# Kernel tuning notes

Hardware: AMD Instinct MI355X
Metric: run time of the kernel (lower is better)

The kernel has to match this reference:

```python
import jax, jax.numpy as jnp
import numpy as np

HID = 768
HEADS = 12
HEAD_LEN = HID // HEADS
SCALE_INV = 1.0 / np.sqrt(HEAD_LEN).astype(np.float32)


def setup_inputs() -> dict:
    key = jax.random.key(0)
    ks = jax.random.split(key, 5)
    std = 1.0 / np.sqrt(HID)
    return {
        "x": jax.random.normal(ks[0], (1, 4096, HID), dtype=jnp.float32),
        "w_q": jax.random.normal(ks[1], (HID, HID), dtype=jnp.float32) * std,
        "w_k": jax.random.normal(ks[2], (HID, HID), dtype=jnp.float32) * std,
        "w_v": jax.random.normal(ks[3], (HID, HID), dtype=jnp.float32) * std,
        "w_fc": jax.random.normal(ks[4], (HID, HID), dtype=jnp.float32) * std,
    }


def reference(x, w_q, w_k, w_v, w_fc):
    B, S, D = x.shape
    # torch Linear weight layout [out, in]: y = x @ W.T
    def proj_heads(w):
        y = jnp.einsum("bsd,ed->bse", x, w)
        return y.reshape(B, S, HEADS, HEAD_LEN).transpose(0, 2, 1, 3)  # bhsd
    q = proj_heads(w_q)
    k = proj_heads(w_k)
    v = proj_heads(w_v)
    scores = SCALE_INV * jnp.einsum("bhqd,bhkd->bhqk", q, k)
    attn = jax.nn.softmax(scores, axis=-1)
    out = jnp.einsum("bhqk,bhkd->bhqd", attn, v)
    out = out.transpose(0, 2, 1, 3).reshape(B, S, D)
    return jnp.einsum("bsd,ed->bse", out, w_fc)
```

## Files before the change

kernel.cpp:

```cpp
#include <hip/hip_runtime.h>
#include <hip/hip_bf16.h>

#define S_LEN 4096
#define HID 768
#define NHEAD 12
#define HL 64

typedef __attribute__((ext_vector_type(8))) short short8;
typedef __attribute__((ext_vector_type(4))) float f32x4;
using bf16 = __hip_bfloat16;

__device__ __forceinline__ void gl2lds16(const void* g, void* l) {
  __builtin_amdgcn_global_load_lds((__attribute__((address_space(1))) void*)(g),
                                   (__attribute__((address_space(3))) void*)(l),
                                   16, 0, 0);
}

__device__ __forceinline__ f32x4 mfma_bf16(short8 a, short8 b, f32x4 c) {
  return __builtin_amdgcn_mfma_f32_16x16x32_bf16(a, b, c, 0, 0, 0);
}

__device__ __forceinline__ void storeC(float* C, long idx, float v) { C[idx] = v; }
__device__ __forceinline__ void storeC(bf16* C, long idx, float v) { C[idx] = __float2bfloat16(v); }

#define BAR() asm volatile("s_waitcnt lgkmcnt(0)\n\ts_barrier" ::: "memory")

__global__ __launch_bounds__(256) void cvt_all(
    const float* __restrict__ x, const float* __restrict__ wq,
    const float* __restrict__ wk, const float* __restrict__ wv,
    const float* __restrict__ wfc, bf16* __restrict__ xb, bf16* __restrict__ wqb,
    bf16* __restrict__ wkb, bf16* __restrict__ wvb, bf16* __restrict__ wfcb) {
  const long NX = (long)S_LEN * HID;
  const long NW = (long)HID * HID;
  long i = ((long)blockIdx.x * 256 + threadIdx.x) * 4;
  const float* src;
  bf16* dst;
  long off;
  if (i < NX) {
    src = x; dst = xb; off = i;
  } else {
    long j = i - NX;
    int wsel = (int)(j / NW);
    off = j - (long)wsel * NW;
    src = wsel == 0 ? wq : wsel == 1 ? wk : wsel == 2 ? wv : wfc;
    dst = wsel == 0 ? wqb : wsel == 1 ? wkb : wsel == 2 ? wvb : wfcb;
  }
  float4 v = *(const float4*)(src + off);
  bf16 h0 = __float2bfloat16(v.x), h1 = __float2bfloat16(v.y);
  bf16 h2 = __float2bfloat16(v.z), h3 = __float2bfloat16(v.w);
  ushort4 o;
  o.x = *(unsigned short*)&h0; o.y = *(unsigned short*)&h1;
  o.z = *(unsigned short*)&h2; o.w = *(unsigned short*)&h3;
  *(ushort4*)(dst + off) = o;
}

template <typename OT>
__global__ __launch_bounds__(256) void gemm_bt(
    const bf16* __restrict__ A, const bf16* __restrict__ B0,
    const bf16* __restrict__ B1, const bf16* __restrict__ B2,
    OT* __restrict__ C0, OT* __restrict__ C1, OT* __restrict__ C2, float qscale) {
  constexpr int K = HID;
  __shared__ __align__(16) bf16 As[128 * 32];
  __shared__ __align__(16) bf16 Bs[128 * 32];
  const int z = blockIdx.z;
  const bf16* B = (z == 0) ? B0 : (z == 1) ? B1 : B2;
  OT* C = (z == 0) ? C0 : (z == 1) ? C1 : C2;
  const float sc = (z == 0) ? qscale : 1.0f;
  const int bm = blockIdx.y, bn = blockIdx.x;
  const int t = threadIdx.x, lane = t & 63, w = t >> 6;
  const int wm = w >> 1, wn = w & 1;
  const int q4 = lane >> 4, c16 = lane & 15;
  const int srow = lane >> 2, scol = (lane & 3) * 8;
  const bf16* Ab = A + (long)bm * 128 * K;
  const bf16* Bb = B + (long)bn * 128 * K;
  f32x4 acc[4][4] = {};
  for (int k0 = 0; k0 < K; k0 += 32) {
#pragma unroll
    for (int r = 0; r < 2; ++r) {
      int rowb = r * 64 + w * 16;
      gl2lds16(Ab + (long)(rowb + srow) * K + k0 + scol, &As[rowb * 32]);
      gl2lds16(Bb + (long)(rowb + srow) * K + k0 + scol, &Bs[rowb * 32]);
    }
    __syncthreads();
    short8 af[4], bfv[4];
#pragma unroll
    for (int i = 0; i < 4; ++i)
      af[i] = *(const short8*)&As[(wm * 64 + i * 16 + c16) * 32 + q4 * 8];
#pragma unroll
    for (int j = 0; j < 4; ++j)
      bfv[j] = *(const short8*)&Bs[(wn * 64 + j * 16 + c16) * 32 + q4 * 8];
#pragma unroll
    for (int i = 0; i < 4; ++i)
#pragma unroll
      for (int j = 0; j < 4; ++j)
        acc[i][j] = mfma_bf16(af[i], bfv[j], acc[i][j]);
    __syncthreads();
  }
  const long crow0 = (long)bm * 128 + wm * 64;
  const int ccol0 = bn * 128 + wn * 64;
#pragma unroll
  for (int i = 0; i < 4; ++i)
#pragma unroll
    for (int j = 0; j < 4; ++j)
#pragma unroll
      for (int r = 0; r < 4; ++r) {
        long row = crow0 + i * 16 + q4 * 4 + r;
        int col = ccol0 + j * 16 + c16;
        storeC(C, row * HID + col, sc * acc[i][j][r]);
      }
}

__global__ __launch_bounds__(256) void gemm_fc(const bf16* __restrict__ A,
                                               const bf16* __restrict__ B,
                                               float* __restrict__ C) {
  __shared__ __align__(16) bf16 As[128 * 32];
  __shared__ __align__(16) bf16 Bs[64 * 32];
  const int bm = blockIdx.y, bn = blockIdx.x;
  const int t = threadIdx.x, lane = t & 63, w = t >> 6;
  const int q4 = lane >> 4, c16 = lane & 15;
  const int srow = lane >> 2, scol = (lane & 3) * 8;
  const bf16* Ab = A + (long)bm * 128 * HID;
  const bf16* Bb = B + (long)bn * 64 * HID;
  f32x4 acc[2][4] = {};
  for (int k0 = 0; k0 < HID; k0 += 32) {
#pragma unroll
    for (int r = 0; r < 2; ++r) {
      int rowb = w * 32 + r * 16;
      gl2lds16(Ab + (long)(rowb + srow) * HID + k0 + scol, &As[rowb * 32]);
    }
    gl2lds16(Bb + (long)(w * 16 + srow) * HID + k0 + scol, &Bs[w * 16 * 32]);
    __syncthreads();
    short8 af[2], bfv[4];
#pragma unroll
    for (int i = 0; i < 2; ++i)
      af[i] = *(const short8*)&As[(w * 32 + i * 16 + c16) * 32 + q4 * 8];
#pragma unroll
    for (int j = 0; j < 4; ++j)
      bfv[j] = *(const short8*)&Bs[(j * 16 + c16) * 32 + q4 * 8];
#pragma unroll
    for (int i = 0; i < 2; ++i)
#pragma unroll
      for (int j = 0; j < 4; ++j)
        acc[i][j] = mfma_bf16(af[i], bfv[j], acc[i][j]);
    __syncthreads();
  }
#pragma unroll
  for (int i = 0; i < 2; ++i)
#pragma unroll
    for (int j = 0; j < 4; ++j)
#pragma unroll
      for (int r = 0; r < 4; ++r) {
        long row = (long)bm * 128 + w * 32 + i * 16 + q4 * 4 + r;
        int col = bn * 64 + j * 16 + c16;
        C[row * HID + col] = acc[i][j][r];
      }
}

__global__ __launch_bounds__(256) void transpose_v(const bf16* __restrict__ V,
                                                   bf16* __restrict__ Vt) {
  __shared__ unsigned short tile[64][65];
  const int bs = blockIdx.x * 64;
  const int be = blockIdx.y * 64;
  const int t = threadIdx.x;
#pragma unroll
  for (int p = 0; p < 4; ++p) {
    int i = p * 256 + t;
    int r = i >> 4;
    int c = (i & 15) * 4;
    ushort4 v = *(const ushort4*)((const unsigned short*)V + (long)(bs + r) * HID + be + c);
    tile[r][c] = v.x; tile[r][c + 1] = v.y; tile[r][c + 2] = v.z; tile[r][c + 3] = v.w;
  }
  __syncthreads();
#pragma unroll
  for (int p = 0; p < 4; ++p) {
    int i = p * 256 + t;
    int r = i >> 4;
    int c = (i & 15) * 4;
    ushort4 v;
    v.x = tile[c][r]; v.y = tile[c + 1][r]; v.z = tile[c + 2][r]; v.w = tile[c + 3][r];
    *(ushort4*)((unsigned short*)Vt + (long)(be + r) * S_LEN + bs + c) = v;
  }
}

__global__ __launch_bounds__(256, 3) void flash_attn(const bf16* __restrict__ Q,
                                                     const bf16* __restrict__ Kg,
                                                     const bf16* __restrict__ Vt,
                                                     bf16* __restrict__ O) {
  __shared__ __align__(16) bf16 Ps[2][64 * 128];
  __shared__ float Lred[4][64];
  const int qt = blockIdx.x, h = blockIdx.y;
  const int t = threadIdx.x, lane = t & 63, w = t >> 6;
  const int q4 = lane >> 4, c16 = lane & 15;
  const int s0 = qt * 64;

  short8 qf[2][4];
  {
    const bf16* Qb = Q + (long)(s0 + c16) * HID + h * HL + q4 * 8;
#pragma unroll
    for (int j = 0; j < 4; ++j)
#pragma unroll
      for (int ks = 0; ks < 2; ++ks)
        qf[ks][j] = *(const short8*)(Qb + (long)j * 16 * HID + ks * 32);
  }
  const bf16* kp = Kg + (long)(w * 32 + c16) * HID + h * HL + q4 * 8;
  const bf16* vp = Vt + (long)(h * HL + w * 16 + c16) * S_LEN + q4 * 8;

  float l_part[4] = {0.f, 0.f, 0.f, 0.f};
  f32x4 o_acc[4] = {};
  short8 kf[2][2], vf[4];
#pragma unroll
  for (int rr = 0; rr < 2; ++rr)
#pragma unroll
    for (int ks = 0; ks < 2; ++ks)
      kf[rr][ks] = *(const short8*)(kp + (long)rr * 16 * HID + ks * 32);
#pragma unroll
  for (int kc = 0; kc < 4; ++kc) vf[kc] = *(const short8*)(vp + kc * 32);

  for (int kt = 0; kt < S_LEN / 128; ++kt) {
    bf16* Pb = Ps[kt & 1];
    f32x4 sacc[2][4] = {};
#pragma unroll
    for (int rr = 0; rr < 2; ++rr)
#pragma unroll
      for (int ks = 0; ks < 2; ++ks)
#pragma unroll
        for (int j = 0; j < 4; ++j)
          sacc[rr][j] = mfma_bf16(kf[rr][ks], qf[ks][j], sacc[rr][j]);

    const bf16* kpn = (kt == S_LEN / 128 - 1) ? kp : kp + 128 * HID;
#pragma unroll
    for (int rr = 0; rr < 2; ++rr)
#pragma unroll
      for (int ks = 0; ks < 2; ++ks)
        kf[rr][ks] = *(const short8*)(kpn + (long)rr * 16 * HID + ks * 32);
    kp = kpn;

#pragma unroll
    for (int rr = 0; rr < 2; ++rr) {
      const int wch = ((w * 4 + rr * 2 + (q4 >> 1)));
#pragma unroll
      for (int j = 0; j < 4; ++j) {
        float p0 = __builtin_amdgcn_exp2f(sacc[rr][j][0]);
        float p1 = __builtin_amdgcn_exp2f(sacc[rr][j][1]);
        float p2 = __builtin_amdgcn_exp2f(sacc[rr][j][2]);
        float p3 = __builtin_amdgcn_exp2f(sacc[rr][j][3]);
        l_part[j] += (p0 + p1) + (p2 + p3);
        __hip_bfloat162 a01 = __float22bfloat162_rn(float2{p0, p1});
        __hip_bfloat162 a23 = __float22bfloat162_rn(float2{p2, p3});
        int2 pk;
        pk.x = *(int*)&a01;
        pk.y = *(int*)&a23;
        *(int2*)&Pb[(j * 16 + c16) * 128 + (wch ^ c16) * 8 + (q4 & 1) * 4] = pk;
      }
    }
    BAR();

#pragma unroll
    for (int kc = 0; kc < 4; ++kc) {
#pragma unroll
      for (int j = 0; j < 4; ++j) {
        short8 pf = *(const short8*)&Pb[(j * 16 + c16) * 128 + ((kc * 4 + q4) ^ c16) * 8];
        o_acc[j] = mfma_bf16(vf[kc], pf, o_acc[j]);
      }
    }
    const bf16* vpn = (kt == S_LEN / 128 - 1) ? vp : vp + 128;
#pragma unroll
    for (int kc = 0; kc < 4; ++kc) vf[kc] = *(const short8*)(vpn + kc * 32);
    vp = vpn;
  }

#pragma unroll
  for (int j = 0; j < 4; ++j) {
    float s = l_part[j];
    s += __shfl_xor(s, 16, 64);
    s += __shfl_xor(s, 32, 64);
    Lred[w][j * 16 + c16] = s;
  }
  __syncthreads();
#pragma unroll
  for (int j = 0; j < 4; ++j) {
    int q = j * 16 + c16;
    float lt = Lred[0][q] + Lred[1][q] + Lred[2][q] + Lred[3][q];
    float rl = 1.0f / lt;
    float v0 = o_acc[j][0] * rl, v1 = o_acc[j][1] * rl;
    float v2 = o_acc[j][2] * rl, v3 = o_acc[j][3] * rl;
    bf16 b0 = __float2bfloat16(v0), b1 = __float2bfloat16(v1);
    bf16 b2 = __float2bfloat16(v2), b3 = __float2bfloat16(v3);
    short4 pk;
    pk.x = *(short*)&b0; pk.y = *(short*)&b1; pk.z = *(short*)&b2; pk.w = *(short*)&b3;
    *(short4*)&O[(long)(s0 + q) * HID + h * HL + w * 16 + q4 * 4] = pk;
  }
}

extern "C" void kernel_launch(void* const* d_in, const int* in_sizes, int n_in,
                              void* d_out, int out_size, void* d_ws, size_t ws_size,
                              hipStream_t stream) {
  const float* x = (const float*)d_in[0];
  const float* wq = (const float*)d_in[1];
  const float* wk = (const float*)d_in[2];
  const float* wv = (const float*)d_in[3];
  const float* wfc = (const float*)d_in[4];
  float* out = (float*)d_out;

  const long NBIG = (long)S_LEN * HID * sizeof(bf16);
  const long NWB = (long)HID * HID * sizeof(bf16);
  char* p = (char*)d_ws;
  bf16* xb = (bf16*)p;   p += NBIG;
  bf16* wqb = (bf16*)p;  p += NWB;
  bf16* wkb = (bf16*)p;  p += NWB;
  bf16* wvb = (bf16*)p;  p += NWB;
  bf16* wfcb = (bf16*)p; p += NWB;
  bf16* Qb = (bf16*)p;   p += NBIG;
  bf16* Kb = (bf16*)p;   p += NBIG;
  bf16* Vb = (bf16*)p;   p += NBIG;
  bf16* Vtb = (bf16*)p;  p += NBIG;
  bf16* Ob = (bf16*)p;   p += NBIG;

  const float c1 = 0.125f * 1.44269504088896340736f;

  const long total4 = ((long)S_LEN * HID + 4L * HID * HID) / 4;
  cvt_all<<<(int)(total4 / 256), 256, 0, stream>>>(x, wq, wk, wv, wfc, xb, wqb, wkb,
                                                   wvb, wfcb);
  gemm_bt<bf16><<<dim3(HID / 128, S_LEN / 128, 3), 256, 0, stream>>>(
      xb, wqb, wkb, wvb, Qb, Kb, Vb, c1);
  transpose_v<<<dim3(S_LEN / 64, HID / 64), 256, 0, stream>>>(Vb, Vtb);
  flash_attn<<<dim3(S_LEN / 64, NHEAD), 256, 0, stream>>>(Qb, Kb, Vtb, Ob);
  gemm_fc<<<dim3(HID / 64, S_LEN / 128), 256, 0, stream>>>(Ob, wfcb, out);
}
```

Before: 211.0 us.

## Triple-buffer LDS in projection GEMMs with async prefetch and smaller fc tiles

Both bf16 GEMMs now keep three LDS buffers and issue global-to-LDS loads two k-steps ahead. Each step uses a single barrier that waits on vmcnt instead of two __syncthreads, so loads can overlap MFMA work. The output GEMM also switches to 64x64 tiles on a 2x2 wave grid, doubling its block count for better CU coverage. The cost is more LDS per block and a hand-tuned vmcnt wait count that has to match the number of outstanding loads.

```diff
diff --git a/kernel.cpp b/kernel.cpp
--- a/kernel.cpp
+++ b/kernel.cpp
@@ -24,6 +24,8 @@
 __device__ __forceinline__ void storeC(bf16* C, long idx, float v) { C[idx] = __float2bfloat16(v); }
 
 #define BAR() asm volatile("s_waitcnt lgkmcnt(0)\n\ts_barrier" ::: "memory")
+#define BAR_VM(n) \
+  asm volatile("s_waitcnt vmcnt(" #n ") lgkmcnt(0)\n\ts_barrier" ::: "memory")
 
 __global__ __launch_bounds__(256) void cvt_all(
     const float* __restrict__ x, const float* __restrict__ wq,
@@ -55,13 +57,13 @@
 }
 
 template <typename OT>
-__global__ __launch_bounds__(256) void gemm_bt(
+__global__ __launch_bounds__(256, 3) void gemm_bt(
     const bf16* __restrict__ A, const bf16* __restrict__ B0,
     const bf16* __restrict__ B1, const bf16* __restrict__ B2,
     OT* __restrict__ C0, OT* __restrict__ C1, OT* __restrict__ C2, float qscale) {
-  constexpr int K = HID;
-  __shared__ __align__(16) bf16 As[128 * 32];
-  __shared__ __align__(16) bf16 Bs[128 * 32];
+  constexpr int K = HID, NK = K / 32;
+  __shared__ __align__(16) bf16 As[3][128 * 32];
+  __shared__ __align__(16) bf16 Bs[3][128 * 32];
   const int z = blockIdx.z;
   const bf16* B = (z == 0) ? B0 : (z == 1) ? B1 : B2;
   OT* C = (z == 0) ? C0 : (z == 1) ? C1 : C2;
@@ -73,28 +75,36 @@
   const int srow = lane >> 2, scol = (lane & 3) * 8;
   const bf16* Ab = A + (long)bm * 128 * K;
   const bf16* Bb = B + (long)bn * 128 * K;
-  f32x4 acc[4][4] = {};
-  for (int k0 = 0; k0 < K; k0 += 32) {
+
+  auto stage = [&](int k, int buf) {
 #pragma unroll
     for (int r = 0; r < 2; ++r) {
       int rowb = r * 64 + w * 16;
-      gl2lds16(Ab + (long)(rowb + srow) * K + k0 + scol, &As[rowb * 32]);
-      gl2lds16(Bb + (long)(rowb + srow) * K + k0 + scol, &Bs[rowb * 32]);
+      gl2lds16(Ab + (long)(rowb + srow) * K + k * 32 + scol, &As[buf][rowb * 32]);
+      gl2lds16(Bb + (long)(rowb + srow) * K + k * 32 + scol, &Bs[buf][rowb * 32]);
     }
-    __syncthreads();
+  };
+
+  f32x4 acc[4][4] = {};
+  stage(0, 0);
+  stage(1, 1);
+  for (int k = 0; k < NK; ++k) {
+    if (k < NK - 1) BAR_VM(4); else BAR_VM(0);
+    if (k + 2 < NK) stage(k + 2, (k + 2) % 3);
+    const bf16* Al = As[k % 3];
+    const bf16* Bl = Bs[k % 3];
     short8 af[4], bfv[4];
 #pragma unroll
     for (int i = 0; i < 4; ++i)
-      af[i] = *(const short8*)&As[(wm * 64 + i * 16 + c16) * 32 + q4 * 8];
+      af[i] = *(const short8*)&Al[(wm * 64 + i * 16 + c16) * 32 + q4 * 8];
 #pragma unroll
     for (int j = 0; j < 4; ++j)
-      bfv[j] = *(const short8*)&Bs[(wn * 64 + j * 16 + c16) * 32 + q4 * 8];
+      bfv[j] = *(const short8*)&Bl[(wn * 64 + j * 16 + c16) * 32 + q4 * 8];
 #pragma unroll
     for (int i = 0; i < 4; ++i)
 #pragma unroll
       for (int j = 0; j < 4; ++j)
         acc[i][j] = mfma_bf16(af[i], bfv[j], acc[i][j]);
-    __syncthreads();
   }
   const long crow0 = (long)bm * 128 + wm * 64;
   const int ccol0 = bn * 128 + wn * 64;
@@ -110,48 +120,56 @@
       }
 }
 
-__global__ __launch_bounds__(256) void gemm_fc(const bf16* __restrict__ A,
-                                               const bf16* __restrict__ B,
-                                               float* __restrict__ C) {
-  __shared__ __align__(16) bf16 As[128 * 32];
-  __shared__ __align__(16) bf16 Bs[64 * 32];
+__global__ __launch_bounds__(256, 3) void gemm_fc(const bf16* __restrict__ A,
+                                                  const bf16* __restrict__ B,
+                                                  float* __restrict__ C) {
+  constexpr int NK = HID / 32;
+  __shared__ __align__(16) bf16 As[3][64 * 32];
+  __shared__ __align__(16) bf16 Bs[3][64 * 32];
   const int bm = blockIdx.y, bn = blockIdx.x;
   const int t = threadIdx.x, lane = t & 63, w = t >> 6;
+  const int wm = w >> 1, wn = w & 1;
   const int q4 = lane >> 4, c16 = lane & 15;
   const int srow = lane >> 2, scol = (lane & 3) * 8;
-  const bf16* Ab = A + (long)bm * 128 * HID;
+  const bf16* Ab = A + (long)bm * 64 * HID;
   const bf16* Bb = B + (long)bn * 64 * HID;
-  f32x4 acc[2][4] = {};
-  for (int k0 = 0; k0 < HID; k0 += 32) {
-#pragma unroll
-    for (int r = 0; r < 2; ++r) {
-      int rowb = w * 32 + r * 16;
-      gl2lds16(Ab + (long)(rowb + srow) * HID + k0 + scol, &As[rowb * 32]);
-    }
-    gl2lds16(Bb + (long)(w * 16 + srow) * HID + k0 + scol, &Bs[w * 16 * 32]);
-    __syncthreads();
-    short8 af[2], bfv[4];
+
+  auto stage = [&](int k, int buf) {
+    gl2lds16(Ab + (long)(w * 16 + srow) * HID + k * 32 + scol,
+             &As[buf][w * 16 * 32]);
+    gl2lds16(Bb + (long)(w * 16 + srow) * HID + k * 32 + scol,
+             &Bs[buf][w * 16 * 32]);
+  };
+
+  f32x4 acc[2][2] = {};
+  stage(0, 0);
+  stage(1, 1);
+  for (int k = 0; k < NK; ++k) {
+    if (k < NK - 1) BAR_VM(2); else BAR_VM(0);
+    if (k + 2 < NK) stage(k + 2, (k + 2) % 3);
+    const bf16* Al = As[k % 3];
+    const bf16* Bl = Bs[k % 3];
+    short8 af[2], bfv[2];
 #pragma unroll
     for (int i = 0; i < 2; ++i)
-      af[i] = *(const short8*)&As[(w * 32 + i * 16 + c16) * 32 + q4 * 8];
-#pragma unroll
-    for (int j = 0; j < 4; ++j)
-      bfv[j] = *(const short8*)&Bs[(j * 16 + c16) * 32 + q4 * 8];
+      af[i] = *(const short8*)&Al[(wm * 32 + i * 16 + c16) * 32 + q4 * 8];
+#pragma unroll
+    for (int j = 0; j < 2; ++j)
+      bfv[j] = *(const short8*)&Bl[(wn * 32 + j * 16 + c16) * 32 + q4 * 8];
 #pragma unroll
     for (int i = 0; i < 2; ++i)
 #pragma unroll
-      for (int j = 0; j < 4; ++j)
+      for (int j = 0; j < 2; ++j)
         acc[i][j] = mfma_bf16(af[i], bfv[j], acc[i][j]);
-    __syncthreads();
   }
 #pragma unroll
   for (int i = 0; i < 2; ++i)
 #pragma unroll
-    for (int j = 0; j < 4; ++j)
+    for (int j = 0; j < 2; ++j)
 #pragma unroll
       for (int r = 0; r < 4; ++r) {
-        long row = (long)bm * 128 + w * 32 + i * 16 + q4 * 4 + r;
-        int col = bn * 64 + j * 16 + c16;
+        long row = (long)bm * 64 + wm * 32 + i * 16 + q4 * 4 + r;
+        int col = bn * 64 + wn * 32 + j * 16 + c16;
         C[row * HID + col] = acc[i][j][r];
       }
 }
@@ -325,5 +343,5 @@
       xb, wqb, wkb, wvb, Qb, Kb, Vb, c1);
   transpose_v<<<dim3(S_LEN / 64, HID / 64), 256, 0, stream>>>(Vb, Vtb);
   flash_attn<<<dim3(S_LEN / 64, NHEAD), 256, 0, stream>>>(Qb, Kb, Vtb, Ob);
-  gemm_fc<<<dim3(HID / 64, S_LEN / 128), 256, 0, stream>>>(Ob, wfcb, out);
-}
+  gemm_fc<<<dim3(HID / 64, S_LEN / 64), 256, 0, stream>>>(Ob, wfcb, out);
+}
```

Result: no change. 213.3 us (+1.1%).

## Fuse all stages into one persistent kernel with software grid barriers

Applied to the files above, without the earlier changes.

Merges the conversion, QKV projection, V transpose, flash attention and output projection into a single 768-block kernel separated by atomic-counter grid barriers. It removes launch gaps and the separate transpose pass by writing V transposed from the projection epilogue through LDS. GEMM tiles are retiled (128x96 for QKV, 64x64 for FC) to match the fixed block count. The software grid barrier needs all 768 blocks co-resident (3 per CU at launch bounds 3), which could deadlock if occupancy falls short, and the smaller FC tiles reduce data reuse.

```diff
diff --git a/kernel.cpp b/kernel.cpp
--- a/kernel.cpp
+++ b/kernel.cpp
@@ -5,6 +5,7 @@
 #define HID 768
 #define NHEAD 12
 #define HL 64
+#define NBLK 768u
 
 typedef __attribute__((ext_vector_type(8))) short short8;
 typedef __attribute__((ext_vector_type(4))) float f32x4;
@@ -20,275 +21,283 @@
   return __builtin_amdgcn_mfma_f32_16x16x32_bf16(a, b, c, 0, 0, 0);
 }
 
-__device__ __forceinline__ void storeC(float* C, long idx, float v) { C[idx] = v; }
-__device__ __forceinline__ void storeC(bf16* C, long idx, float v) { C[idx] = __float2bfloat16(v); }
-
 #define BAR() asm volatile("s_waitcnt lgkmcnt(0)\n\ts_barrier" ::: "memory")
 
-__global__ __launch_bounds__(256) void cvt_all(
+__device__ __forceinline__ void gridbar(unsigned* cnt, int idx) {
+  __syncthreads();
+  __threadfence();
+  if (threadIdx.x == 0) {
+    atomicAdd(&cnt[idx], 1u);
+    while (__hip_atomic_load(&cnt[idx], __ATOMIC_RELAXED,
+                             __HIP_MEMORY_SCOPE_AGENT) < NBLK)
+      __builtin_amdgcn_s_sleep(8);
+  }
+  __syncthreads();
+  __threadfence();
+}
+
+__global__ __launch_bounds__(256, 3) void mha_mega(
     const float* __restrict__ x, const float* __restrict__ wq,
     const float* __restrict__ wk, const float* __restrict__ wv,
-    const float* __restrict__ wfc, bf16* __restrict__ xb, bf16* __restrict__ wqb,
-    bf16* __restrict__ wkb, bf16* __restrict__ wvb, bf16* __restrict__ wfcb) {
-  const long NX = (long)S_LEN * HID;
-  const long NW = (long)HID * HID;
-  long i = ((long)blockIdx.x * 256 + threadIdx.x) * 4;
-  const float* src;
-  bf16* dst;
-  long off;
-  if (i < NX) {
-    src = x; dst = xb; off = i;
-  } else {
-    long j = i - NX;
-    int wsel = (int)(j / NW);
-    off = j - (long)wsel * NW;
-    src = wsel == 0 ? wq : wsel == 1 ? wk : wsel == 2 ? wv : wfc;
-    dst = wsel == 0 ? wqb : wsel == 1 ? wkb : wsel == 2 ? wvb : wfcb;
-  }
-  float4 v = *(const float4*)(src + off);
-  bf16 h0 = __float2bfloat16(v.x), h1 = __float2bfloat16(v.y);
-  bf16 h2 = __float2bfloat16(v.z), h3 = __float2bfloat16(v.w);
-  ushort4 o;
-  o.x = *(unsigned short*)&h0; o.y = *(unsigned short*)&h1;
-  o.z = *(unsigned short*)&h2; o.w = *(unsigned short*)&h3;
-  *(ushort4*)(dst + off) = o;
-}
-
-template <typename OT>
-__global__ __launch_bounds__(256) void gemm_bt(
-    const bf16* __restrict__ A, const bf16* __restrict__ B0,
-    const bf16* __restrict__ B1, const bf16* __restrict__ B2,
-    OT* __restrict__ C0, OT* __restrict__ C1, OT* __restrict__ C2, float qscale) {
-  constexpr int K = HID;
-  __shared__ __align__(16) bf16 As[128 * 32];
-  __shared__ __align__(16) bf16 Bs[128 * 32];
-  const int z = blockIdx.z;
-  const bf16* B = (z == 0) ? B0 : (z == 1) ? B1 : B2;
-  OT* C = (z == 0) ? C0 : (z == 1) ? C1 : C2;
-  const float sc = (z == 0) ? qscale : 1.0f;
-  const int bm = blockIdx.y, bn = blockIdx.x;
-  const int t = threadIdx.x, lane = t & 63, w = t >> 6;
-  const int wm = w >> 1, wn = w & 1;
-  const int q4 = lane >> 4, c16 = lane & 15;
-  const int srow = lane >> 2, scol = (lane & 3) * 8;
-  const bf16* Ab = A + (long)bm * 128 * K;
-  const bf16* Bb = B + (long)bn * 128 * K;
-  f32x4 acc[4][4] = {};
-  for (int k0 = 0; k0 < K; k0 += 32) {
-#pragma unroll
-    for (int r = 0; r < 2; ++r) {
-      int rowb = r * 64 + w * 16;
-      gl2lds16(Ab + (long)(rowb + srow) * K + k0 + scol, &As[rowb * 32]);
-      gl2lds16(Bb + (long)(rowb + srow) * K + k0 + scol, &Bs[rowb * 32]);
-    }
-    __syncthreads();
-    short8 af[4], bfv[4];
-#pragma unroll
-    for (int i = 0; i < 4; ++i)
-      af[i] = *(const short8*)&As[(wm * 64 + i * 16 + c16) * 32 + q4 * 8];
-#pragma unroll
-    for (int j = 0; j < 4; ++j)
-      bfv[j] = *(const short8*)&Bs[(wn * 64 + j * 16 + c16) * 32 + q4 * 8];
-#pragma unroll
-    for (int i = 0; i < 4; ++i)
-#pragma unroll
-      for (int j = 0; j < 4; ++j)
-        acc[i][j] = mfma_bf16(af[i], bfv[j], acc[i][j]);
-    __syncthreads();
-  }
-  const long crow0 = (long)bm * 128 + wm * 64;
-  const int ccol0 = bn * 128 + wn * 64;
-#pragma unroll
-  for (int i = 0; i < 4; ++i)
-#pragma unroll
-    for (int j = 0; j < 4; ++j)
-#pragma unroll
-      for (int r = 0; r < 4; ++r) {
-        long row = crow0 + i * 16 + q4 * 4 + r;
-        int col = ccol0 + j * 16 + c16;
-        storeC(C, row * HID + col, sc * acc[i][j][r]);
-      }
-}
-
-__global__ __launch_bounds__(256) void gemm_fc(const bf16* __restrict__ A,
-                                               const bf16* __restrict__ B,
-                                               float* __restrict__ C) {
-  __shared__ __align__(16) bf16 As[128 * 32];
-  __shared__ __align__(16) bf16 Bs[64 * 32];
-  const int bm = blockIdx.y, bn = blockIdx.x;
+    const float* __restrict__ wfc, bf16* __restrict__ xb,
+    bf16* __restrict__ wqb, bf16* __restrict__ wkb, bf16* __restrict__ wvb,
+    bf16* __restrict__ wfcb, bf16* __restrict__ Qb, bf16* __restrict__ Kb,
+    bf16* __restrict__ Vtb, bf16* __restrict__ Ob, float* __restrict__ out,
+    unsigned* __restrict__ cnt) {
+  __shared__ __align__(16) char SMEM[33792];
+  const int b = blockIdx.x;
   const int t = threadIdx.x, lane = t & 63, w = t >> 6;
   const int q4 = lane >> 4, c16 = lane & 15;
-  const int srow = lane >> 2, scol = (lane & 3) * 8;
-  const bf16* Ab = A + (long)bm * 128 * HID;
-  const bf16* Bb = B + (long)bn * 64 * HID;
-  f32x4 acc[2][4] = {};
-  for (int k0 = 0; k0 < HID; k0 += 32) {
-#pragma unroll
-    for (int r = 0; r < 2; ++r) {
-      int rowb = w * 32 + r * 16;
-      gl2lds16(Ab + (long)(rowb + srow) * HID + k0 + scol, &As[rowb * 32]);
-    }
-    gl2lds16(Bb + (long)(w * 16 + srow) * HID + k0 + scol, &Bs[w * 16 * 32]);
+  const float c1 = 0.125f * 1.44269504088896340736f;
+
+  {
+    const long NX4 = (long)S_LEN * HID / 4;
+    const long NW4 = (long)HID * HID / 4;
+#pragma unroll
+    for (int i = 0; i < 7; ++i) {
+      long g = (long)i * 196608 + (long)b * 256 + t;
+      const float4* src;
+      ushort4* dst;
+      long off;
+      if (g < NX4) {
+        src = (const float4*)x; dst = (ushort4*)xb; off = g;
+      } else {
+        long j = g - NX4;
+        int zz = (int)(j / NW4);
+        off = j - (long)zz * NW4;
+        src = (const float4*)(zz == 0 ? wq : zz == 1 ? wk : zz == 2 ? wv : wfc);
+        dst = (ushort4*)(zz == 0 ? wqb : zz == 1 ? wkb : zz == 2 ? wvb : wfcb);
+      }
+      float4 v = src[off];
+      bf16 h0 = __float2bfloat16(v.x), h1 = __float2bfloat16(v.y);
+      bf16 h2 = __float2bfloat16(v.z), h3 = __float2bfloat16(v.w);
+      ushort4 o;
+      o.x = *(unsigned short*)&h0; o.y = *(unsigned short*)&h1;
+      o.z = *(unsigned short*)&h2; o.w = *(unsigned short*)&h3;
+      dst[off] = o;
+    }
+  }
+  gridbar(cnt, 0);
+
+  {
+    bf16* As = (bf16*)SMEM;
+    bf16* Bs = (bf16*)(SMEM + 128 * 32 * 2);
+    const int z = b >> 8, r8 = b & 255, bn = r8 & 7, bm = r8 >> 3;
+    const bf16* A = xb + (long)bm * 128 * HID;
+    const bf16* Bw = (z == 0 ? wqb : z == 1 ? wkb : wvb) + (long)bn * 96 * HID;
+    const int wm = w >> 1, wn = w & 1;
+    const int srow = lane >> 2, scol = (lane & 3) * 8;
+    f32x4 acc[4][3] = {};
+    for (int k0 = 0; k0 < HID; k0 += 32) {
+      gl2lds16(A + (long)(w * 16 + srow) * HID + k0 + scol, &As[w * 16 * 32]);
+      gl2lds16(A + (long)(64 + w * 16 + srow) * HID + k0 + scol,
+               &As[(64 + w * 16) * 32]);
+      gl2lds16(Bw + (long)(w * 16 + srow) * HID + k0 + scol, &Bs[w * 16 * 32]);
+      if (w < 2)
+        gl2lds16(Bw + (long)(64 + w * 16 + srow) * HID + k0 + scol,
+                 &Bs[(64 + w * 16) * 32]);
+      __syncthreads();
+      short8 af[4], bfv[3];
+#pragma unroll
+      for (int i = 0; i < 4; ++i)
+        af[i] = *(const short8*)&As[(wm * 64 + i * 16 + c16) * 32 + q4 * 8];
+#pragma unroll
+      for (int j = 0; j < 3; ++j)
+        bfv[j] = *(const short8*)&Bs[(wn * 48 + j * 16 + c16) * 32 + q4 * 8];
+#pragma unroll
+      for (int i = 0; i < 4; ++i)
+#pragma unroll
+        for (int j = 0; j < 3; ++j)
+          acc[i][j] = mfma_bf16(af[i], bfv[j], acc[i][j]);
+      __syncthreads();
+    }
+    if (z < 2) {
+      bf16* C = (z == 0) ? Qb : Kb;
+      const float sc = (z == 0) ? c1 : 1.0f;
+#pragma unroll
+      for (int i = 0; i < 4; ++i)
+#pragma unroll
+        for (int j = 0; j < 3; ++j)
+#pragma unroll
+          for (int r = 0; r < 4; ++r) {
+            long row = (long)bm * 128 + wm * 64 + i * 16 + q4 * 4 + r;
+            int col = bn * 96 + wn * 48 + j * 16 + c16;
+            C[row * HID + col] = __float2bfloat16(sc * acc[i][j][r]);
+          }
+    } else {
+      bf16* Lt = (bf16*)SMEM;
+#pragma unroll
+      for (int i = 0; i < 4; ++i)
+#pragma unroll
+        for (int j = 0; j < 3; ++j) {
+          bf16 b0 = __float2bfloat16(acc[i][j][0]);
+          bf16 b1 = __float2bfloat16(acc[i][j][1]);
+          bf16 b2 = __float2bfloat16(acc[i][j][2]);
+          bf16 b3 = __float2bfloat16(acc[i][j][3]);
+          short4 pk;
+          pk.x = *(short*)&b0; pk.y = *(short*)&b1;
+          pk.z = *(short*)&b2; pk.w = *(short*)&b3;
+          *(short4*)&Lt[(wn * 48 + j * 16 + c16) * 136 + wm * 64 + i * 16 +
+                        q4 * 4] = pk;
+        }
+      __syncthreads();
+#pragma unroll
+      for (int p = 0; p < 6; ++p) {
+        int e = p * 16 + (t >> 4);
+        int s = (t & 15) * 8;
+        short8 vv = *(const short8*)&Lt[e * 136 + s];
+        *(short8*)&Vtb[(long)(bn * 96 + e) * S_LEN + bm * 128 + s] = vv;
+      }
+    }
+  }
+  gridbar(cnt, 1);
+
+  {
+    bf16* Ps0 = (bf16*)SMEM;
+    float* Lred = (float*)(SMEM + 32768);
+    const int qt = b & 63, h = b >> 6;
+    const int s0 = qt * 64;
+
+    short8 qf[2][4];
+    {
+      const bf16* Qp = Qb + (long)(s0 + c16) * HID + h * HL + q4 * 8;
+#pragma unroll
+      for (int j = 0; j < 4; ++j)
+#pragma unroll
+        for (int ks = 0; ks < 2; ++ks)
+          qf[ks][j] = *(const short8*)(Qp + (long)j * 16 * HID + ks * 32);
+    }
+    const bf16* kp = Kb + (long)(w * 32 + c16) * HID + h * HL + q4 * 8;
+    const bf16* vp = Vtb + (long)(h * HL + w * 16 + c16) * S_LEN + q4 * 8;
+
+    float l_part[4] = {0.f, 0.f, 0.f, 0.f};
+    f32x4 o_acc[4] = {};
+    short8 kf[2][2], vf[4];
+#pragma unroll
+    for (int rr = 0; rr < 2; ++rr)
+#pragma unroll
+      for (int ks = 0; ks < 2; ++ks)
+        kf[rr][ks] = *(const short8*)(kp + (long)rr * 16 * HID + ks * 32);
+#pragma unroll
+    for (int kc = 0; kc < 4; ++kc) vf[kc] = *(const short8*)(vp + kc * 32);
+
+    for (int kt = 0; kt < S_LEN / 128; ++kt) {
+      bf16* Pb = Ps0 + (kt & 1) * 64 * 128;
+      f32x4 sacc[2][4] = {};
+#pragma unroll
+      for (int rr = 0; rr < 2; ++rr)
+#pragma unroll
+        for (int ks = 0; ks < 2; ++ks)
+#pragma unroll
+          for (int j = 0; j < 4; ++j)
+            sacc[rr][j] = mfma_bf16(kf[rr][ks], qf[ks][j], sacc[rr][j]);
+
+      const bf16* kpn = (kt == S_LEN / 128 - 1) ? kp : kp + 128 * HID;
+#pragma unroll
+      for (int rr = 0; rr < 2; ++rr)
+#pragma unroll
+        for (int ks = 0; ks < 2; ++ks)
+          kf[rr][ks] = *(const short8*)(kpn + (long)rr * 16 * HID + ks * 32);
+      kp = kpn;
+
+#pragma unroll
+      for (int rr = 0; rr < 2; ++rr) {
+        const int wch = (w * 4 + rr * 2 + (q4 >> 1));
+#pragma unroll
+        for (int j = 0; j < 4; ++j) {
+          float p0 = __builtin_amdgcn_exp2f(sacc[rr][j][0]);
+          float p1 = __builtin_amdgcn_exp2f(sacc[rr][j][1]);
+          float p2 = __builtin_amdgcn_exp2f(sacc[rr][j][2]);
+          float p3 = __builtin_amdgcn_exp2f(sacc[rr][j][3]);
+          l_part[j] += (p0 + p1) + (p2 + p3);
+          __hip_bfloat162 a01 = __float22bfloat162_rn(float2{p0, p1});
+          __hip_bfloat162 a23 = __float22bfloat162_rn(float2{p2, p3});
+          int2 pk;
+          pk.x = *(int*)&a01;
+          pk.y = *(int*)&a23;
+          *(int2*)&Pb[(j * 16 + c16) * 128 + (wch ^ c16) * 8 + (q4 & 1) * 4] = pk;
+        }
+      }
+      BAR();
+
+#pragma unroll
+      for (int kc = 0; kc < 4; ++kc) {
+#pragma unroll
+        for (int j = 0; j < 4; ++j) {
+          short8 pf = *(const short8*)&Pb[(j * 16 + c16) * 128 +
+                                          ((kc * 4 + q4) ^ c16) * 8];
+          o_acc[j] = mfma_bf16(vf[kc], pf, o_acc[j]);
+        }
+      }
+      const bf16* vpn = (kt == S_LEN / 128 - 1) ? vp : vp + 128;
+#pragma unroll
+      for (int kc = 0; kc < 4; ++kc) vf[kc] = *(const short8*)(vpn + kc * 32);
+      vp = vpn;
+    }
+
+#pragma unroll
+    for (int j = 0; j < 4; ++j) {
+      float s = l_part[j];
+      s += __shfl_xor(s, 16, 64);
+      s += __shfl_xor(s, 32, 64);
+      Lred[w * 64 + j * 16 + c16] = s;
+    }
     __syncthreads();
-    short8 af[2], bfv[4];
+#pragma unroll
+    for (int j = 0; j < 4; ++j) {
+      int q = j * 16 + c16;
+      float lt = Lred[0 * 64 + q] + Lred[1 * 64 + q] + Lred[2 * 64 + q] +
+                 Lred[3 * 64 + q];
+      float rl = 1.0f / lt;
+      float v0 = o_acc[j][0] * rl, v1 = o_acc[j][1] * rl;
+      float v2 = o_acc[j][2] * rl, v3 = o_acc[j][3] * rl;
+      bf16 b0 = __float2bfloat16(v0), b1 = __float2bfloat16(v1);
+      bf16 b2 = __float2bfloat16(v2), b3 = __float2bfloat16(v3);
+      short4 pk;
+      pk.x = *(short*)&b0; pk.y = *(short*)&b1;
+      pk.z = *(short*)&b2; pk.w = *(short*)&b3;
+      *(short4*)&Ob[(long)(s0 + q) * HID + h * HL + w * 16 + q4 * 4] = pk;
+    }
+  }
+  gridbar(cnt, 2);
+
+  {
+    bf16* As = (bf16*)SMEM;
+    bf16* Bs = (bf16*)(SMEM + 64 * 32 * 2);
+    const int bn = b % 12, bm = b / 12;
+    const bf16* A = Ob + (long)bm * 64 * HID;
+    const bf16* Bw = wfcb + (long)bn * 64 * HID;
+    const int wm = w >> 1, wn = w & 1;
+    const int srow = lane >> 2, scol = (lane & 3) * 8;
+    f32x4 acc[2][2] = {};
+    for (int k0 = 0; k0 < HID; k0 += 32) {
+      gl2lds16(A + (long)(w * 16 + srow) * HID + k0 + scol, &As[w * 16 * 32]);
+      gl2lds16(Bw + (long)(w * 16 + srow) * HID + k0 + scol, &Bs[w * 16 * 32]);
+      __syncthreads();
+      short8 af[2], bfv[2];
+#pragma unroll
+      for (int i = 0; i < 2; ++i)
+        af[i] = *(const short8*)&As[(wm * 32 + i * 16 + c16) * 32 + q4 * 8];
+#pragma unroll
+      for (int j = 0; j < 2; ++j)
+        bfv[j] = *(const short8*)&Bs[(wn * 32 + j * 16 + c16) * 32 + q4 * 8];
+#pragma unroll
+      for (int i = 0; i < 2; ++i)
+#pragma unroll
+        for (int j = 0; j < 2; ++j)
+          acc[i][j] = mfma_bf16(af[i], bfv[j], acc[i][j]);
+      __syncthreads();
+    }
 #pragma unroll
     for (int i = 0; i < 2; ++i)
-      af[i] = *(const short8*)&As[(w * 32 + i * 16 + c16) * 32 + q4 * 8];
-#pragma unroll
-    for (int j = 0; j < 4; ++j)
-      bfv[j] = *(const short8*)&Bs[(j * 16 + c16) * 32 + q4 * 8];
-#pragma unroll
-    for (int i = 0; i < 2; ++i)
-#pragma unroll
-      for (int j = 0; j < 4; ++j)
-        acc[i][j] = mfma_bf16(af[i], bfv[j], acc[i][j]);
-    __syncthreads();
-  }
-#pragma unroll
-  for (int i = 0; i < 2; ++i)
-#pragma unroll
-    for (int j = 0; j < 4; ++j)
-#pragma unroll
-      for (int r = 0; r < 4; ++r) {
-        long row = (long)bm * 128 + w * 32 + i * 16 + q4 * 4 + r;
-        int col = bn * 64 + j * 16 + c16;
-        C[row * HID + col] = acc[i][j][r];
-      }
-}
-
-__global__ __launch_bounds__(256) void transpose_v(const bf16* __restrict__ V,
-                                                   bf16* __restrict__ Vt) {
-  __shared__ unsigned short tile[64][65];
-  const int bs = blockIdx.x * 64;
-  const int be = blockIdx.y * 64;
-  const int t = threadIdx.x;
-#pragma unroll
-  for (int p = 0; p < 4; ++p) {
-    int i = p * 256 + t;
-    int r = i >> 4;
-    int c = (i & 15) * 4;
-    ushort4 v = *(const ushort4*)((const unsigned short*)V + (long)(bs + r) * HID + be + c);
-    tile[r][c] = v.x; tile[r][c + 1] = v.y; tile[r][c + 2] = v.z; tile[r][c + 3] = v.w;
-  }
-  __syncthreads();
-#pragma unroll
-  for (int p = 0; p < 4; ++p) {
-    int i = p * 256 + t;
-    int r = i >> 4;
-    int c = (i & 15) * 4;
-    ushort4 v;
-    v.x = tile[c][r]; v.y = tile[c + 1][r]; v.z = tile[c + 2][r]; v.w = tile[c + 3][r];
-    *(ushort4*)((unsigned short*)Vt + (long)(be + r) * S_LEN + bs + c) = v;
-  }
-}
-
-__global__ __launch_bounds__(256, 3) void flash_attn(const bf16* __restrict__ Q,
-                                                     const bf16* __restrict__ Kg,
-                                                     const bf16* __restrict__ Vt,
-                                                     bf16* __restrict__ O) {
-  __shared__ __align__(16) bf16 Ps[2][64 * 128];
-  __shared__ float Lred[4][64];
-  const int qt = blockIdx.x, h = blockIdx.y;
-  const int t = threadIdx.x, lane = t & 63, w = t >> 6;
-  const int q4 = lane >> 4, c16 = lane & 15;
-  const int s0 = qt * 64;
-
-  short8 qf[2][4];
-  {
-    const bf16* Qb = Q + (long)(s0 + c16) * HID + h * HL + q4 * 8;
-#pragma unroll
-    for (int j = 0; j < 4; ++j)
-#pragma unroll
-      for (int ks = 0; ks < 2; ++ks)
-        qf[ks][j] = *(const short8*)(Qb + (long)j * 16 * HID + ks * 32);
-  }
-  const bf16* kp = Kg + (long)(w * 32 + c16) * HID + h * HL + q4 * 8;
-  const bf16* vp = Vt + (long)(h * HL + w * 16 + c16) * S_LEN + q4 * 8;
-
-  float l_part[4] = {0.f, 0.f, 0.f, 0.f};
-  f32x4 o_acc[4] = {};
-  short8 kf[2][2], vf[4];
-#pragma unroll
-  for (int rr = 0; rr < 2; ++rr)
-#pragma unroll
-    for (int ks = 0; ks < 2; ++ks)
-      kf[rr][ks] = *(const short8*)(kp + (long)rr * 16 * HID + ks * 32);
-#pragma unroll
-  for (int kc = 0; kc < 4; ++kc) vf[kc] = *(const short8*)(vp + kc * 32);
-
-  for (int kt = 0; kt < S_LEN / 128; ++kt) {
-    bf16* Pb = Ps[kt & 1];
-    f32x4 sacc[2][4] = {};
-#pragma unroll
-    for (int rr = 0; rr < 2; ++rr)
-#pragma unroll
-      for (int ks = 0; ks < 2; ++ks)
-#pragma unroll
-        for (int j = 0; j < 4; ++j)
-          sacc[rr][j] = mfma_bf16(kf[rr][ks], qf[ks][j], sacc[rr][j]);
-
-    const bf16* kpn = (kt == S_LEN / 128 - 1) ? kp : kp + 128 * HID;
-#pragma unroll
-    for (int rr = 0; rr < 2; ++rr)
-#pragma unroll
-      for (int ks = 0; ks < 2; ++ks)
-        kf[rr][ks] = *(const short8*)(kpn + (long)rr * 16 * HID + ks * 32);
-    kp = kpn;
-
-#pragma unroll
-    for (int rr = 0; rr < 2; ++rr) {
-      const int wch = ((w * 4 + rr * 2 + (q4 >> 1)));
-#pragma unroll
-      for (int j = 0; j < 4; ++j) {
-        float p0 = __builtin_amdgcn_exp2f(sacc[rr][j][0]);
-        float p1 = __builtin_amdgcn_exp2f(sacc[rr][j][1]);
-        float p2 = __builtin_amdgcn_exp2f(sacc[rr][j][2]);
-        float p3 = __builtin_amdgcn_exp2f(sacc[rr][j][3]);
-        l_part[j] += (p0 + p1) + (p2 + p3);
-        __hip_bfloat162 a01 = __float22bfloat162_rn(float2{p0, p1});
-        __hip_bfloat162 a23 = __float22bfloat162_rn(float2{p2, p3});
-        int2 pk;
-        pk.x = *(int*)&a01;
-        pk.y = *(int*)&a23;
-        *(int2*)&Pb[(j * 16 + c16) * 128 + (wch ^ c16) * 8 + (q4 & 1) * 4] = pk;
-      }
-    }
-    BAR();
-
-#pragma unroll
-    for (int kc = 0; kc < 4; ++kc) {
-#pragma unroll
-      for (int j = 0; j < 4; ++j) {
-        short8 pf = *(const short8*)&Pb[(j * 16 + c16) * 128 + ((kc * 4 + q4) ^ c16) * 8];
-        o_acc[j] = mfma_bf16(vf[kc], pf, o_acc[j]);
-      }
-    }
-    const bf16* vpn = (kt == S_LEN / 128 - 1) ? vp : vp + 128;
-#pragma unroll
-    for (int kc = 0; kc < 4; ++kc) vf[kc] = *(const short8*)(vpn + kc * 32);
-    vp = vpn;
-  }
-
-#pragma unroll
-  for (int j = 0; j < 4; ++j) {
-    float s = l_part[j];
-    s += __shfl_xor(s, 16, 64);
-    s += __shfl_xor(s, 32, 64);
-    Lred[w][j * 16 + c16] = s;
-  }
-  __syncthreads();
-#pragma unroll
-  for (int j = 0; j < 4; ++j) {
-    int q = j * 16 + c16;
-    float lt = Lred[0][q] + Lred[1][q] + Lred[2][q] + Lred[3][q];
-    float rl = 1.0f / lt;
-    float v0 = o_acc[j][0] * rl, v1 = o_acc[j][1] * rl;
-    float v2 = o_acc[j][2] * rl, v3 = o_acc[j][3] * rl;
-    bf16 b0 = __float2bfloat16(v0), b1 = __float2bfloat16(v1);
-    bf16 b2 = __float2bfloat16(v2), b3 = __float2bfloat16(v3);
-    short4 pk;
-    pk.x = *(short*)&b0; pk.y = *(short*)&b1; pk.z = *(short*)&b2; pk.w = *(short*)&b3;
-    *(short4*)&O[(long)(s0 + q) * HID + h * HL + w * 16 + q4 * 4] = pk;
+#pragma unroll
+      for (int j = 0; j < 2; ++j)
+#pragma unroll
+        for (int r = 0; r < 4; ++r) {
+          long row = (long)bm * 64 + wm * 32 + i * 16 + q4 * 4 + r;
+          int col = bn * 64 + wn * 32 + j * 16 + c16;
+          out[row * HID + col] = acc[i][j][r];
+        }
   }
 }
 
@@ -305,6 +314,7 @@
   const long NBIG = (long)S_LEN * HID * sizeof(bf16);
   const long NWB = (long)HID * HID * sizeof(bf16);
   char* p = (char*)d_ws;
+  unsigned* cnt = (unsigned*)p; p += 256;
   bf16* xb = (bf16*)p;   p += NBIG;
   bf16* wqb = (bf16*)p;  p += NWB;
   bf16* wkb = (bf16*)p;  p += NWB;
@@ -312,18 +322,10 @@
   bf16* wfcb = (bf16*)p; p += NWB;
   bf16* Qb = (bf16*)p;   p += NBIG;
   bf16* Kb = (bf16*)p;   p += NBIG;
-  bf16* Vb = (bf16*)p;   p += NBIG;
   bf16* Vtb = (bf16*)p;  p += NBIG;
   bf16* Ob = (bf16*)p;   p += NBIG;
 
-  const float c1 = 0.125f * 1.44269504088896340736f;
-
-  const long total4 = ((long)S_LEN * HID + 4L * HID * HID) / 4;
-  cvt_all<<<(int)(total4 / 256), 256, 0, stream>>>(x, wq, wk, wv, wfc, xb, wqb, wkb,
-                                                   wvb, wfcb);
-  gemm_bt<bf16><<<dim3(HID / 128, S_LEN / 128, 3), 256, 0, stream>>>(
-      xb, wqb, wkb, wvb, Qb, Kb, Vb, c1);
-  transpose_v<<<dim3(S_LEN / 64, HID / 64), 256, 0, stream>>>(Vb, Vtb);
-  flash_attn<<<dim3(S_LEN / 64, NHEAD), 256, 0, stream>>>(Qb, Kb, Vtb, Ob);
-  gemm_fc<<<dim3(HID / 64, S_LEN / 128), 256, 0, stream>>>(Ob, wfcb, out);
-}
+  hipMemsetAsync(cnt, 0, 256, stream);
+  mha_mega<<<NBLK, 256, 0, stream>>>(x, wq, wk, wv, wfc, xb, wqb, wkb, wvb, wfcb,
+                                     Qb, Kb, Vtb, Ob, out, cnt);
+}
```

Result: slower. 728.4 us (+245.2%).
